# Kernel tuning notes

Measured on AMD Instinct MI355X. Metric: run time of the kernel, lower is better.

Reference implementation:

```python
import jax, jax.numpy as jnp
import numpy as np

N_NODES = 100000
N_EDGES = 3200000
N_REL = 16
EMB = 32
N_CLS = 50
BATCH = 1024


def setup_inputs() -> dict:
    key = jax.random.key(0)
    ks = jax.random.split(key, 8)
    return {
        "emb0": jax.random.normal(ks[0], (N_NODES, EMB), dtype=jnp.float32),
        "W1": jax.random.normal(ks[1], (N_REL, EMB, EMB), dtype=jnp.float32),
        "W2": jax.random.normal(ks[2], (N_REL, EMB, EMB), dtype=jnp.float32),
        "cls_w": jax.random.normal(ks[3], (N_CLS, EMB), dtype=jnp.float32),
        "cls_b": jax.random.normal(ks[4], (N_CLS,), dtype=jnp.float32),
        "src": jax.random.randint(ks[5], (N_EDGES,), 0, N_NODES, dtype=jnp.int64) if jax.config.jax_enable_x64 else jax.random.randint(ks[5], (N_EDGES,), 0, N_NODES).astype(jnp.int64),
        "rel": jax.random.randint(ks[6], (N_EDGES,), 0, N_REL).astype(jnp.int64),
        "dst": jax.random.randint(ks[7], (N_EDGES,), 0, N_NODES).astype(jnp.int64),
        "b": BATCH,
    }


def reference(emb0, W1, W2, cls_w, cls_b, src, rel, dst, b):
    n, e = emb0.shape
    r = W1.shape[0]
    # fr = src + n * rel : row index of the (r*n, n) sparse adjacency, per SimpleRGCN
    fr = (src + n * rel).astype(jnp.int32)
    dst_i = dst.astype(jnp.int32)
    # util.sum_sparse: normalize each edge by the sum over its row (out-degree per (rel, src))
    deg = jax.ops.segment_sum(jnp.ones((fr.shape[0],), dtype=emb0.dtype), fr, num_segments=r * n)
    vals = 1.0 / deg[fr]  # [E]; only evaluated at rows with >=1 edge

    def rgcn_layer(h, W):
        # util.spmm: output[fr] += vals * h[dst]  -> (r*n, e)
        msgs = vals[:, None] * h[dst_i]                       # [E, e]
        agg = jax.ops.segment_sum(msgs, fr, num_segments=r * n)
        agg = agg.reshape(r, n, e)                            # [r, n, e]
        # einsum('rij, rnj -> nri').sum(dim=1) == einsum('rij, rnj -> ni')
        return jax.nn.relu(jnp.einsum('rij,rnj->ni', W, agg))

    h = rgcn_layer(emb0, W1)
    h = rgcn_layer(h, W2)
    pooled = h[:b]                                            # batch entities occupy first b slots
    return pooled @ cls_w.T + cls_b
```

## Files before the change

### kernel.cpp

```cpp
#include <hip/hip_runtime.h>
#include <stdint.h>

#define N_NODES 100000
#define N_EDGES 3200000
#define N_REL   16
#define NBKT    391
#define NBLK    256
#define EPB     12500
#define NPGB    200
#define BKT_PAD 3856
#define PADDED_E (N_EDGES + 16 + NBKT * BKT_PAD)
#define PAD_FLAG 0x80000000u

typedef __attribute__((ext_vector_type(8))) short  short8;
typedef __attribute__((ext_vector_type(4))) short  short4_t;
typedef __attribute__((ext_vector_type(4))) float  f32x4;

static __device__ __forceinline__ int align16i(int x) { return (x + 15) & ~15; }

static __device__ __forceinline__ unsigned short f32_to_bf16(float f) {
    union { float f; unsigned int u; } v; v.f = f;
    unsigned int u = v.u;
    unsigned int r = u + 0x7FFFu + ((u >> 16) & 1u);
    return (unsigned short)(r >> 16);
}
static __device__ __forceinline__ float bf2f(unsigned short s) {
    union { unsigned int u; float f; } cv; cv.u = ((unsigned int)s) << 16;
    return cv.f;
}

__global__ __launch_bounds__(512) void k_histA(const int* __restrict__ src,
                                               int* __restrict__ table) {
    __shared__ int lh[NBKT];
    int tid = threadIdx.x, bid = blockIdx.x;
    for (int t = tid; t < NBKT; t += 512) lh[t] = 0;
    __syncthreads();
    int e0 = bid * EPB;
    for (int e = e0 + tid; e < e0 + EPB; e += 512)
        atomicAdd(&lh[src[e] >> 8], 1);
    __syncthreads();
    for (int t = tid; t < NBKT; t += 512) table[bid * NBKT + t] = lh[t];
}

__global__ void k_btot(const int* __restrict__ table, int* __restrict__ btot) {
    int b = blockIdx.x * 256 + threadIdx.x;
    if (b >= NBKT) return;
    int s = 0;
    for (int k = 0; k < NBLK; ++k) s += table[k * NBKT + b];
    btot[b] = s;
}

__global__ void k_bbase(const int* __restrict__ btot, int* __restrict__ bktbase) {
    __shared__ int sd[512];
    int tid = threadIdx.x;
    int v = (tid < NBKT) ? btot[tid] : 0;
    sd[tid] = v; __syncthreads();
    int x = v;
    for (int off = 1; off < 512; off <<= 1) {
        int t = (tid >= off) ? sd[tid - off] : 0;
        __syncthreads();
        x += t; sd[tid] = x;
        __syncthreads();
    }
    if (tid < NBKT) bktbase[tid] = x - v;
    if (tid == 0) bktbase[NBKT] = N_EDGES;
}

__global__ void k_goff(const int* __restrict__ table, const int* __restrict__ bktbase,
                       int* __restrict__ goff) {
    __shared__ int sd[NBLK];
    int b = blockIdx.x;
    int tid = threadIdx.x;
    int v = table[tid * NBKT + b];
    sd[tid] = v; __syncthreads();
    int x = v;
    for (int off = 1; off < NBLK; off <<= 1) {
        int t = (tid >= off) ? sd[tid - off] : 0;
        __syncthreads();
        x += t; sd[tid] = x;
        __syncthreads();
    }
    int bp = align16i(bktbase[b]) + b * BKT_PAD;
    goff[tid * NBKT + b] = bp + (x - v);
}

__global__ __launch_bounds__(512) void k_partB_pgemm(const int* __restrict__ src,
                                                     const int* __restrict__ rel,
                                                     const int* __restrict__ dst,
                                                     const int* __restrict__ goff,
                                                     unsigned int* __restrict__ part,
                                                     const float* __restrict__ emb0,
                                                     const float* __restrict__ W1,
                                                     unsigned short* __restrict__ P) {
    __shared__ int lcur[NBKT];
    __shared__ unsigned short wlds[512 * 32];
    int tid = threadIdx.x, bid = blockIdx.x;
    if (bid < NBLK) {
        for (int t = tid; t < NBKT; t += 512) lcur[t] = goff[bid * NBKT + t];
        __syncthreads();
        int e0 = bid * EPB;
        for (int e = e0 + tid; e < e0 + EPB; e += 512) {
            int s = src[e];
            int pos = atomicAdd(&lcur[s >> 8], 1);
            part[pos] = ((unsigned)(s & 255) << 21) | ((unsigned)rel[e] << 17) | (unsigned)dst[e];
        }
    } else {
        int pb = bid - NBLK;
        for (int t = tid; t < 4096; t += 512) {
            f32x4 v = ((const f32x4*)W1)[t];
            short4_t o;
#pragma unroll
            for (int e = 0; e < 4; ++e) o[e] = (short)f32_to_bf16(v[e]);
            ((short4_t*)wlds)[t] = o;
        }
        __syncthreads();
        int gw   = pb * 8 + (tid >> 6);
        int lane = tid & 63;
        int col16 = lane & 15, krow = lane >> 4;
        const int NTILES = N_NODES / 16;
        for (int tile = gw; tile < NTILES; tile += NPGB * 8) {
            int n0 = tile * 16;
            const float* ap = emb0 + (size_t)(n0 + col16) * 32 + krow * 8;
            f32x4 a0 = *(const f32x4*)ap;
            f32x4 a1 = *(const f32x4*)(ap + 4);
            short8 b;
#pragma unroll
            for (int e = 0; e < 4; ++e) { b[e] = (short)f32_to_bf16(a0[e]); b[e + 4] = (short)f32_to_bf16(a1[e]); }
#pragma unroll
            for (int rcb = 0; rcb < 32; ++rcb) {
                short8 a = *(const short8*)&wlds[(size_t)(rcb * 16 + col16) * 32 + krow * 8];
                f32x4 c = {0.f, 0.f, 0.f, 0.f};
                c = __builtin_amdgcn_mfma_f32_16x16x32_bf16(a, b, c, 0, 0, 0);
                short4_t o;
#pragma unroll
                for (int reg = 0; reg < 4; ++reg) o[reg] = (short)f32_to_bf16(c[reg]);
                *(short4_t*)(P + (size_t)(n0 + col16) * 512 + rcb * 16 + krow * 4) = o;
            }
        }
    }
}

__global__ __launch_bounds__(256) void k_place(const unsigned int* __restrict__ part,
                                               const int* __restrict__ bktbase,
                                               unsigned int* __restrict__ sorted_rd,
                                               int* __restrict__ sorted_src,
                                               int* __restrict__ offs,
                                               int* __restrict__ cnt,
                                               float* __restrict__ inv2) {
    __shared__ int lhist[256 * 16];
    __shared__ int sd[256];
    __shared__ int lcur[256];
    int b = blockIdx.x, tid = threadIdx.x;
    int n0 = b << 8;
    int braw = bktbase[b];
    int bsize = bktbase[b + 1] - braw;
    int bp = align16i(braw) + b * BKT_PAD;
    int bp_next = align16i(bktbase[b + 1]) + (b + 1) * BKT_PAD;
#pragma unroll
    for (int k = 0; k < 16; ++k) lhist[tid + k * 256] = 0;
    __syncthreads();
    for (int t = bp + tid; t < bp + bsize; t += 256)
        atomicAdd(&lhist[part[t] >> 17], 1);
    __syncthreads();
    int ncnt = 0;
#pragma unroll
    for (int r = 0; r < 16; ++r) ncnt += lhist[(tid << 4) | r];
    int ncnt_p = align16i(ncnt);
    sd[tid] = ncnt_p; __syncthreads();
    int x = ncnt_p;
    for (int off = 1; off < 256; off <<= 1) {
        int t = (tid >= off) ? sd[tid - off] : 0;
        __syncthreads();
        x += t; sd[tid] = x;
        __syncthreads();
    }
    int nodeoff = bp + (x - ncnt_p);
    lcur[tid] = nodeoff;
    int node = n0 + tid;
    if (node < N_NODES) { offs[node] = nodeoff; cnt[node] = ncnt; }
    for (int t = tid; t < 4096; t += 256) {
        int nd = n0 + (t >> 4);
        if (nd < N_NODES) {
            int c = lhist[t];
            inv2[((size_t)nd << 4) + (t & 15)] = c ? 1.0f / (float)c : 0.f;
        }
    }
    __syncthreads();
    for (int t = bp + tid; t < bp + bsize; t += 256) {
        unsigned int v = part[t];
        int j = (int)(v >> 21);
        int p = atomicAdd(&lcur[j], 1);
        sorted_rd[p] = v & 0x1FFFFFu;
        if (b < 4) sorted_src[p] = n0 + j;
    }
    __syncthreads();
    for (int p = nodeoff + ncnt; p < nodeoff + ncnt_p; ++p) sorted_rd[p] = PAD_FLAG;
    int content_end = bp + sd[255];
    for (int t = content_end + tid; t < bp_next; t += 256) sorted_rd[t] = PAD_FLAG;
}

__global__ __launch_bounds__(256) void k_agg1(const unsigned int* __restrict__ sorted_rd,
                                              const int* __restrict__ offs,
                                              const int* __restrict__ cnt,
                                              const float* __restrict__ inv2,
                                              const unsigned short* __restrict__ P,
                                              float* __restrict__ h1) {
    int node = blockIdx.x * 4 + (threadIdx.x >> 6);
    int lane = threadIdx.x & 63;
    int i = lane & 31, h = lane >> 5;
    int start = offs[node];
    int ecp = align16i(cnt[node]);
    const float* ivn = inv2 + ((size_t)node << 4);
    float acc = 0.f;
    for (int t0 = start + h * 16; t0 < start + ecp; t0 += 32) {
        uint4 qa = *reinterpret_cast<const uint4*>(sorted_rd + t0);
        uint4 qb = *reinterpret_cast<const uint4*>(sorted_rd + t0 + 4);
        uint4 qc = *reinterpret_cast<const uint4*>(sorted_rd + t0 + 8);
        uint4 qd = *reinterpret_cast<const uint4*>(sorted_rd + t0 + 12);
        unsigned pk[16] = {qa.x, qa.y, qa.z, qa.w, qb.x, qb.y, qb.z, qb.w,
                           qc.x, qc.y, qc.z, qc.w, qd.x, qd.y, qd.z, qd.w};
        float v[16], val[16];
#pragma unroll
        for (int k = 0; k < 16; ++k) {
            unsigned d = pk[k] & 0x1FFFFu, r = (pk[k] >> 17) & 15u;
            v[k]   = bf2f(P[(size_t)d * 512 + r * 32 + i]);
            val[k] = (pk[k] & PAD_FLAG) ? 0.f : ivn[r];
        }
#pragma unroll
        for (int k = 0; k < 16; ++k) acc += val[k] * v[k];
    }
    acc += __shfl_xor(acc, 32, 64);
    if (h == 0) h1[(size_t)node * 32 + i] = fmaxf(acc, 0.f);
}

__global__ void k_agg2(const unsigned int* __restrict__ sorted_rd,
                       const int* __restrict__ sorted_src,
                       const int* __restrict__ bktbase,
                       const float* __restrict__ inv2, const float* __restrict__ h1,
                       float* __restrict__ agg2) {
    int E2 = ((bktbase[4] + 15) & ~15) + 4 * BKT_PAD;
    long total = (long)E2 * 32;
    long stride = (long)gridDim.x * blockDim.x;
    for (long t = (long)blockIdx.x * blockDim.x + threadIdx.x; t < total; t += stride) {
        int e = (int)(t >> 5), j = (int)(t & 31);
        unsigned int pk = sorted_rd[e];
        if (pk & PAD_FLAG) continue;
        int r = (int)(pk >> 17), d = (int)(pk & 0x1FFFFu);
        int s = sorted_src[e];
        float val = inv2[((size_t)s << 4) + r];
        atomicAdd(&agg2[(s << 9) + (r << 5) + j], val * h1[(size_t)d * 32 + j]);
    }
}

__global__ void k_h2(const float* __restrict__ agg2, const float* __restrict__ W2,
                     float* __restrict__ h2pre) {
    int t = blockIdx.x * 256 + threadIdx.x;
    int s = t >> 5, i = t & 31;
    const float* arow = agg2 + (s << 9);
    float acc = 0.f;
#pragma unroll 4
    for (int r = 0; r < 16; ++r) {
        const float* wrow = W2 + r * 1024 + i * 32;
        const float* a = arow + r * 32;
#pragma unroll
        for (int j = 0; j < 32; ++j) acc += wrow[j] * a[j];
    }
    h2pre[t] = acc;
}

__global__ void k_cls(const float* __restrict__ h2pre, const float* __restrict__ cls_w,
                      const float* __restrict__ cls_b, float* __restrict__ out) {
    int t = blockIdx.x * 256 + threadIdx.x;
    int b = t >> 6, c = t & 63;
    if (b >= 1024 || c >= 50) return;
    float acc = cls_b[c];
#pragma unroll
    for (int j = 0; j < 32; ++j)
        acc += fmaxf(h2pre[b * 32 + j], 0.f) * cls_w[c * 32 + j];
    out[b * 50 + c] = acc;
}

extern "C" void kernel_launch(void* const* d_in, const int* in_sizes, int n_in,
                              void* d_out, int out_size, void* d_ws, size_t ws_size,
                              hipStream_t stream) {
    const float* emb0  = (const float*)d_in[0];
    const float* W1    = (const float*)d_in[1];
    const float* W2    = (const float*)d_in[2];
    const float* cls_w = (const float*)d_in[3];
    const float* cls_b = (const float*)d_in[4];
    const int*   src   = (const int*)d_in[5];
    const int*   rel   = (const int*)d_in[6];
    const int*   dst   = (const int*)d_in[7];
    float* out = (float*)d_out;

    char* ws = (char*)d_ws;
    size_t off = 0;
    auto alloc = [&](size_t bytes) -> void* {
        void* p = ws + off;
        off = (off + bytes + 255) & ~((size_t)255);
        return p;
    };
    float*          inv2       = (float*)alloc((size_t)N_NODES * 16 * 4);
    int*            offs       = (int*)alloc((size_t)N_NODES * 4);
    int*            cnt        = (int*)alloc((size_t)N_NODES * 4);
    int*            table      = (int*)alloc((size_t)NBLK * NBKT * 4);
    int*            btot       = (int*)alloc((size_t)NBKT * 4);
    int*            bktbase    = (int*)alloc((size_t)(NBKT + 1) * 4);
    int*            goff       = (int*)alloc((size_t)NBLK * NBKT * 4);
    unsigned int*   sorted_rd  = (unsigned int*)alloc((size_t)PADDED_E * 4);
    int*            sorted_src = (int*)alloc((size_t)65536 * 4);
    unsigned int*   partX      = (unsigned int*)alloc((size_t)PADDED_E * 4);
    unsigned short* P          = (unsigned short*)alloc((size_t)N_NODES * 512 * 2);
    float*          agg2       = (float*)alloc((size_t)1024 * 512 * 4);
    float*          h2pre      = (float*)alloc((size_t)1024 * 32 * 4);
    unsigned int*   part       = partX;
    float*          h1         = (float*)partX;

    hipMemsetAsync(agg2, 0, (size_t)1024 * 512 * 4, stream);

    k_histA       <<<NBLK, 512, 0, stream>>>(src, table);
    k_btot        <<<2, 256, 0, stream>>>(table, btot);
    k_bbase       <<<1, 512, 0, stream>>>(btot, bktbase);
    k_goff        <<<NBKT, NBLK, 0, stream>>>(table, bktbase, goff);
    k_partB_pgemm <<<NBLK + NPGB, 512, 0, stream>>>(src, rel, dst, goff, part, emb0, W1, P);
    k_place       <<<NBKT, 256, 0, stream>>>(part, bktbase, sorted_rd, sorted_src, offs, cnt, inv2);
    k_agg1        <<<25000, 256, 0, stream>>>(sorted_rd, offs, cnt, inv2, P, h1);
    k_agg2        <<<1024, 256, 0, stream>>>(sorted_rd, sorted_src, bktbase, inv2, h1, agg2);
    k_h2          <<<128, 256, 0, stream>>>(agg2, W2, h2pre);
    k_cls         <<<256, 256, 0, stream>>>(h2pre, cls_w, cls_b, out);
}
```

Measured before the change: 345.6 us.

## Split partition/GEMM kernel, pad weight LDS rows, fuse head and bucket-scan kernels

Merges the bucket-total and prefix-scan kernels into one, and fuses the layer-2 transform with the classifier into a single per-row head kernel. Splits the combined partition+projection kernel into two launches, and the projection GEMM now uses 256-thread blocks with a padded (stride 40) LDS layout for the bf16 weights to avoid bank conflicts. This removes several small launches. In exchange, the partition scatter and the GEMM no longer overlap inside one grid.

```diff
diff --git a/kernel.cpp b/kernel.cpp
--- a/kernel.cpp
+++ b/kernel.cpp
@@ -7,7 +7,6 @@
 #define NBKT    391
 #define NBLK    256
 #define EPB     12500
-#define NPGB    200
 #define BKT_PAD 3856
 #define PADDED_E (N_EDGES + 16 + NBKT * BKT_PAD)
 #define PAD_FLAG 0x80000000u
@@ -42,18 +41,15 @@
     for (int t = tid; t < NBKT; t += 512) table[bid * NBKT + t] = lh[t];
 }
 
-__global__ void k_btot(const int* __restrict__ table, int* __restrict__ btot) {
-    int b = blockIdx.x * 256 + threadIdx.x;
-    if (b >= NBKT) return;
-    int s = 0;
-    for (int k = 0; k < NBLK; ++k) s += table[k * NBKT + b];
-    btot[b] = s;
-}
-
-__global__ void k_bbase(const int* __restrict__ btot, int* __restrict__ bktbase) {
+__global__ __launch_bounds__(512) void k_bb(const int* __restrict__ table,
+                                            int* __restrict__ bktbase) {
     __shared__ int sd[512];
     int tid = threadIdx.x;
-    int v = (tid < NBKT) ? btot[tid] : 0;
+    int v = 0;
+    if (tid < NBKT) {
+#pragma unroll 8
+        for (int k = 0; k < NBLK; ++k) v += table[k * NBKT + tid];
+    }
     sd[tid] = v; __syncthreads();
     int x = v;
     for (int off = 1; off < 512; off <<= 1) {
@@ -84,58 +80,61 @@
     goff[tid * NBKT + b] = bp + (x - v);
 }
 
-__global__ __launch_bounds__(512) void k_partB_pgemm(const int* __restrict__ src,
-                                                     const int* __restrict__ rel,
-                                                     const int* __restrict__ dst,
-                                                     const int* __restrict__ goff,
-                                                     unsigned int* __restrict__ part,
-                                                     const float* __restrict__ emb0,
-                                                     const float* __restrict__ W1,
-                                                     unsigned short* __restrict__ P) {
+__global__ __launch_bounds__(512) void k_partB(const int* __restrict__ src,
+                                               const int* __restrict__ rel,
+                                               const int* __restrict__ dst,
+                                               const int* __restrict__ goff,
+                                               unsigned int* __restrict__ part) {
     __shared__ int lcur[NBKT];
-    __shared__ unsigned short wlds[512 * 32];
     int tid = threadIdx.x, bid = blockIdx.x;
-    if (bid < NBLK) {
-        for (int t = tid; t < NBKT; t += 512) lcur[t] = goff[bid * NBKT + t];
-        __syncthreads();
-        int e0 = bid * EPB;
-        for (int e = e0 + tid; e < e0 + EPB; e += 512) {
-            int s = src[e];
-            int pos = atomicAdd(&lcur[s >> 8], 1);
-            part[pos] = ((unsigned)(s & 255) << 21) | ((unsigned)rel[e] << 17) | (unsigned)dst[e];
-        }
-    } else {
-        int pb = bid - NBLK;
-        for (int t = tid; t < 4096; t += 512) {
-            f32x4 v = ((const f32x4*)W1)[t];
+    for (int t = tid; t < NBKT; t += 512) lcur[t] = goff[bid * NBKT + t];
+    __syncthreads();
+    int e0 = bid * EPB;
+    for (int e = e0 + tid; e < e0 + EPB; e += 512) {
+        int s = src[e];
+        int pos = atomicAdd(&lcur[s >> 8], 1);
+        part[pos] = ((unsigned)(s & 255) << 21) | ((unsigned)rel[e] << 17) | (unsigned)dst[e];
+    }
+}
+
+__global__ __launch_bounds__(256) void k_pgemm(const float* __restrict__ emb0,
+                                               const float* __restrict__ W1,
+                                               unsigned short* __restrict__ P,
+                                               int nwaves) {
+    __shared__ unsigned short wlds[512 * 40];
+    int tid = threadIdx.x;
+    for (int t4 = tid * 4; t4 < 16384; t4 += 1024) {
+        f32x4 v = *(const f32x4*)(W1 + t4);
+        short4_t o;
+#pragma unroll
+        for (int e = 0; e < 4; ++e) o[e] = (short)f32_to_bf16(v[e]);
+        int rc = t4 >> 5, j = t4 & 31;
+        *(short4_t*)&wlds[rc * 40 + j] = o;
+    }
+    __syncthreads();
+
+    int gw   = (blockIdx.x * 256 + tid) >> 6;
+    int lane = tid & 63;
+    int col16 = lane & 15, krow = lane >> 4;
+
+    const int NTILES = N_NODES / 16;
+    for (int tile = gw; tile < NTILES; tile += nwaves) {
+        int n0 = tile * 16;
+        const float* ap = emb0 + (size_t)(n0 + col16) * 32 + krow * 8;
+        f32x4 a0 = *(const f32x4*)ap;
+        f32x4 a1 = *(const f32x4*)(ap + 4);
+        short8 b;
+#pragma unroll
+        for (int e = 0; e < 4; ++e) { b[e] = (short)f32_to_bf16(a0[e]); b[e + 4] = (short)f32_to_bf16(a1[e]); }
+#pragma unroll
+        for (int rcb = 0; rcb < 32; ++rcb) {
+            short8 a = *(const short8*)&wlds[(rcb * 16 + col16) * 40 + krow * 8];
+            f32x4 c = {0.f, 0.f, 0.f, 0.f};
+            c = __builtin_amdgcn_mfma_f32_16x16x32_bf16(a, b, c, 0, 0, 0);
             short4_t o;
 #pragma unroll
-            for (int e = 0; e < 4; ++e) o[e] = (short)f32_to_bf16(v[e]);
-            ((short4_t*)wlds)[t] = o;
-        }
-        __syncthreads();
-        int gw   = pb * 8 + (tid >> 6);
-        int lane = tid & 63;
-        int col16 = lane & 15, krow = lane >> 4;
-        const int NTILES = N_NODES / 16;
-        for (int tile = gw; tile < NTILES; tile += NPGB * 8) {
-            int n0 = tile * 16;
-            const float* ap = emb0 + (size_t)(n0 + col16) * 32 + krow * 8;
-            f32x4 a0 = *(const f32x4*)ap;
-            f32x4 a1 = *(const f32x4*)(ap + 4);
-            short8 b;
-#pragma unroll
-            for (int e = 0; e < 4; ++e) { b[e] = (short)f32_to_bf16(a0[e]); b[e + 4] = (short)f32_to_bf16(a1[e]); }
-#pragma unroll
-            for (int rcb = 0; rcb < 32; ++rcb) {
-                short8 a = *(const short8*)&wlds[(size_t)(rcb * 16 + col16) * 32 + krow * 8];
-                f32x4 c = {0.f, 0.f, 0.f, 0.f};
-                c = __builtin_amdgcn_mfma_f32_16x16x32_bf16(a, b, c, 0, 0, 0);
-                short4_t o;
-#pragma unroll
-                for (int reg = 0; reg < 4; ++reg) o[reg] = (short)f32_to_bf16(c[reg]);
-                *(short4_t*)(P + (size_t)(n0 + col16) * 512 + rcb * 16 + krow * 4) = o;
-            }
+            for (int reg = 0; reg < 4; ++reg) o[reg] = (short)f32_to_bf16(c[reg]);
+            *(short4_t*)(P + (size_t)(n0 + col16) * 512 + rcb * 16 + krow * 4) = o;
         }
     }
 }
@@ -252,32 +251,32 @@
     }
 }
 
-__global__ void k_h2(const float* __restrict__ agg2, const float* __restrict__ W2,
-                     float* __restrict__ h2pre) {
-    int t = blockIdx.x * 256 + threadIdx.x;
-    int s = t >> 5, i = t & 31;
-    const float* arow = agg2 + (s << 9);
-    float acc = 0.f;
+__global__ __launch_bounds__(64) void k_head(const float* __restrict__ agg2,
+                                             const float* __restrict__ W2,
+                                             const float* __restrict__ cls_w,
+                                             const float* __restrict__ cls_b,
+                                             float* __restrict__ out) {
+    __shared__ float hr[32];
+    int s = blockIdx.x, tid = threadIdx.x;
+    if (tid < 32) {
+        const float* arow = agg2 + (s << 9);
+        float acc = 0.f;
 #pragma unroll 4
-    for (int r = 0; r < 16; ++r) {
-        const float* wrow = W2 + r * 1024 + i * 32;
-        const float* a = arow + r * 32;
-#pragma unroll
-        for (int j = 0; j < 32; ++j) acc += wrow[j] * a[j];
-    }
-    h2pre[t] = acc;
-}
-
-__global__ void k_cls(const float* __restrict__ h2pre, const float* __restrict__ cls_w,
-                      const float* __restrict__ cls_b, float* __restrict__ out) {
-    int t = blockIdx.x * 256 + threadIdx.x;
-    int b = t >> 6, c = t & 63;
-    if (b >= 1024 || c >= 50) return;
-    float acc = cls_b[c];
-#pragma unroll
-    for (int j = 0; j < 32; ++j)
-        acc += fmaxf(h2pre[b * 32 + j], 0.f) * cls_w[c * 32 + j];
-    out[b * 50 + c] = acc;
+        for (int r = 0; r < 16; ++r) {
+            const float* wrow = W2 + r * 1024 + tid * 32;
+            const float* a = arow + r * 32;
+#pragma unroll
+            for (int j = 0; j < 32; ++j) acc += wrow[j] * a[j];
+        }
+        hr[tid] = fmaxf(acc, 0.f);
+    }
+    __syncthreads();
+    if (tid < 50) {
+        float acc = cls_b[tid];
+#pragma unroll
+        for (int j = 0; j < 32; ++j) acc += hr[j] * cls_w[tid * 32 + j];
+        out[s * 50 + tid] = acc;
+    }
 }
 
 extern "C" void kernel_launch(void* const* d_in, const int* in_sizes, int n_in,
@@ -304,7 +303,6 @@
     int*            offs       = (int*)alloc((size_t)N_NODES * 4);
     int*            cnt        = (int*)alloc((size_t)N_NODES * 4);
     int*            table      = (int*)alloc((size_t)NBLK * NBKT * 4);
-    int*            btot       = (int*)alloc((size_t)NBKT * 4);
     int*            bktbase    = (int*)alloc((size_t)(NBKT + 1) * 4);
     int*            goff       = (int*)alloc((size_t)NBLK * NBKT * 4);
     unsigned int*   sorted_rd  = (unsigned int*)alloc((size_t)PADDED_E * 4);
@@ -312,20 +310,18 @@
     unsigned int*   partX      = (unsigned int*)alloc((size_t)PADDED_E * 4);
     unsigned short* P          = (unsigned short*)alloc((size_t)N_NODES * 512 * 2);
     float*          agg2       = (float*)alloc((size_t)1024 * 512 * 4);
-    float*          h2pre      = (float*)alloc((size_t)1024 * 32 * 4);
     unsigned int*   part       = partX;
     float*          h1         = (float*)partX;
 
     hipMemsetAsync(agg2, 0, (size_t)1024 * 512 * 4, stream);
 
-    k_histA       <<<NBLK, 512, 0, stream>>>(src, table);
-    k_btot        <<<2, 256, 0, stream>>>(table, btot);
-    k_bbase       <<<1, 512, 0, stream>>>(btot, bktbase);
-    k_goff        <<<NBKT, NBLK, 0, stream>>>(table, bktbase, goff);
-    k_partB_pgemm <<<NBLK + NPGB, 512, 0, stream>>>(src, rel, dst, goff, part, emb0, W1, P);
-    k_place       <<<NBKT, 256, 0, stream>>>(part, bktbase, sorted_rd, sorted_src, offs, cnt, inv2);
-    k_agg1        <<<25000, 256, 0, stream>>>(sorted_rd, offs, cnt, inv2, P, h1);
-    k_agg2        <<<1024, 256, 0, stream>>>(sorted_rd, sorted_src, bktbase, inv2, h1, agg2);
-    k_h2          <<<128, 256, 0, stream>>>(agg2, W2, h2pre);
-    k_cls         <<<256, 256, 0, stream>>>(h2pre, cls_w, cls_b, out);
-}
+    k_histA <<<NBLK, 512, 0, stream>>>(src, table);
+    k_bb    <<<1, 512, 0, stream>>>(table, bktbase);
+    k_goff  <<<NBKT, NBLK, 0, stream>>>(table, bktbase, goff);
+    k_partB <<<NBLK, 512, 0, stream>>>(src, rel, dst, goff, part);
+    k_pgemm <<<391, 256, 0, stream>>>(emb0, W1, P, 391 * 4);
+    k_place <<<NBKT, 256, 0, stream>>>(part, bktbase, sorted_rd, sorted_src, offs, cnt, inv2);
+    k_agg1  <<<25000, 256, 0, stream>>>(sorted_rd, offs, cnt, inv2, P, h1);
+    k_agg2  <<<1024, 256, 0, stream>>>(sorted_rd, sorted_src, bktbase, inv2, h1, agg2);
+    k_head  <<<1024, 64, 0, stream>>>(agg2, W2, cls_w, cls_b, out);
+}
```

After: 336.5 us. 1.03x faster.
